# Optimization experiments

Measured on AMD Instinct MI355X. Metric: run time of the kernel, lower is better.

Reference implementation:

```python
import jax, jax.numpy as jnp
import numpy as np

NC = 6          # num_classes
KP = 8          # num_prototype_per_class
NPROTO = NC * KP
PH, PW = 4, 4   # patch grid (num_h, num_w)
MOM = 0.999
EPS = 1e-6


def _layernorm(x, g, b):
    mu = jnp.mean(x, axis=-1, keepdims=True)
    var = jnp.var(x, axis=-1, keepdims=True)
    return (x - mu) / jnp.sqrt(var + EPS) * g + b


def _patch_split(x, nh, nw):
    # (B,C,H,W) -> (B*nh*nw, C, H//nh, W//nw)
    B, C, H, W = x.shape
    ph, pw = H // nh, W // nw
    x = x.reshape(B, C, nh, ph, nw, pw).transpose(0, 2, 4, 1, 3, 5)
    return x.reshape(B * nh * nw, C, ph, pw)


def setup_inputs() -> dict:
    key = jax.random.key(0)
    k1, k2, k3 = jax.random.split(key, 3)
    B, C, Hh, Wh = 8, 128, 128, 128
    Horg, Worg = 512, 512
    return {
        "feats": jax.random.normal(k1, (B, C, Hh, Wh), dtype=jnp.float32),
        "gt": jax.random.randint(k2, (B, Horg, Worg), 0, 7, dtype=jnp.int64),
        "prototype": jax.random.normal(k3, (NPROTO, C), dtype=jnp.float32),
        "ln1_gamma": jnp.ones((C,), jnp.float32),
        "ln1_beta": jnp.zeros((C,), jnp.float32),
        "ln2_gamma": jnp.ones((NPROTO,), jnp.float32),
        "ln2_beta": jnp.zeros((NPROTO,), jnp.float32),
    }


def reference(feats, gt, prototype, ln1_gamma, ln1_beta, ln2_gamma, ln2_beta):
    B, C, Hh, Wh = feats.shape
    Horg, Worg = gt.shape[1], gt.shape[2]

    # --- nearest-neighbor downsample of gt to head resolution (torch 'nearest')
    ih = (jnp.arange(Hh) * Horg) // Hh
    iw = (jnp.arange(Wh) * Worg) // Wh
    label = gt[:, ih[:, None], iw[None, :]]                      # (B,Hh,Wh)
    mask = (label.astype(jnp.int32) != NC).astype(label.dtype)
    one_hot = jax.nn.one_hot(label * mask, NC, dtype=jnp.float32)  # (B,Hh,Wh,NC)
    # torch code does a raw .view(B,-1,Hh,Wh) on the contiguous one-hot; replicate
    pred0 = one_hot.reshape(B, NC, Hh, Wh)

    # --- patch split + spatial gather (softmax-weighted class centers per patch)
    pf = _patch_split(feats, PH, PW)                             # (B*16, C, ph, pw)
    pp = _patch_split(pred0, PH, PW)                             # (B*16, NC, ph, pw)
    bp = pf.shape[0]
    probs = jax.nn.softmax(pp.reshape(bp, NC, -1), axis=2)       # (B*16, NC, HWp)
    fflat = pf.reshape(bp, C, -1)                                # (B*16, C, HWp)
    ctx = jnp.einsum('bkn,bcn->bkc', probs, fflat)               # (B*16, NC, C)

    centers = ctx.reshape(B, PH * PW, NC, C)
    centers = jax.nn.gelu(_layernorm(centers, ln1_gamma, ln1_beta), approximate=False)
    centers = centers.reshape(B, PH * PW * NC, C)                # (B, 96, C)

    # --- nearest prototype assignment (cdist + argmin)
    c2 = jnp.sum(centers * centers, axis=-1)                     # (B,96)
    p2 = jnp.sum(prototype * prototype, axis=-1)                 # (48,)
    d2 = c2[:, :, None] + p2[None, None, :] - 2.0 * jnp.einsum('bmc,kc->bmk', centers, prototype)
    nearest = jnp.argmin(jnp.sqrt(jnp.maximum(d2, 0.0)), axis=-1)  # (B,96)

    # --- sequential, order-dependent momentum EMA scatter update (training path)
    sg = jax.lax.stop_gradient
    idx_flat = nearest.reshape(-1)
    ctr_flat = sg(centers.reshape(-1, C))

    def step(proto, xs):
        i, v = xs
        nv = MOM * proto[i] + (1.0 - MOM) * v
        return proto.at[i].set(nv), None

    proto_val, _ = jax.lax.scan(step, sg(prototype), (idx_flat, ctr_flat))
    # in torch the update writes .data (no grad); downstream grad w.r.t. prototype is identity
    proto_new = prototype + sg(proto_val - prototype)

    # --- prototype-to-pixel cdist similarity map
    nf = feats.reshape(B, C, -1).transpose(0, 2, 1)              # (B,HW,C)
    f2 = jnp.sum(nf * nf, axis=-1)                               # (B,HW)
    pn2 = jnp.sum(proto_new * proto_new, axis=-1)                # (48,)
    d2b = pn2[None, :, None] + f2[:, None, :] - 2.0 * jnp.einsum('kc,bnc->bkn', proto_new, nf)
    distance_l2 = jnp.sqrt(jnp.maximum(d2b, 0.0))                # (B,48,HW)

    p2c = (1.0 / (1.0 + 2.0 * distance_l2)).reshape(B, NPROTO, Hh, Wh)
    p2c = p2c.transpose(0, 2, 3, 1)
    p2c = jax.nn.gelu(_layernorm(p2c, ln2_gamma, ln2_beta), approximate=False)
    p2c_sim_map = p2c.transpose(0, 3, 1, 2)                      # (B,48,Hh,Wh)

    pred = p2c_sim_map.reshape(B, KP, NC, Hh, Wh).max(axis=1)    # (B,NC,Hh,Wh)
    pred = jax.image.resize(pred, (B, NC, Horg, Worg), method='bilinear')

    prototype_expand = jnp.broadcast_to(proto_new, (B, NPROTO, C))
    return pred, prototype_expand, p2c_sim_map, distance_l2, proto_new
```

## Files before the change

kernel.cpp:

```cpp
#include <hip/hip_runtime.h>
#include <hip/hip_bf16.h>
#include <math.h>


#define E_M1 1.71828182845904523536f
#define INV_SQRT2 0.70710678118654752440f

typedef float v2f __attribute__((ext_vector_type(2)));

__device__ __forceinline__ float gelu_exact(float x) {
    return 0.5f * x * (1.f + erff(x * INV_SQRT2));
}
__device__ __forceinline__ v2f splat2(float x) { v2f r; r.x = x; r.y = x; return r; }

__global__ __launch_bounds__(256) void kern0b(const int* __restrict__ gt,
                                              unsigned char* __restrict__ maskb) {
    int idx = blockIdx.x * 256 + threadIdx.x;
    int b = idx >> 14, P = idx & 16383;
    const int* gb = gt + b * 262144;
    unsigned int m = 0;
    #pragma unroll
    for (int c = 0; c < 6; ++c) {
        int pos = c * 16384 + P;
        int hp = pos / 768;
        int rem = pos - hp * 768;
        int wp = rem / 6;
        int kp = rem - wp * 6;
        int g = gb[(4 * hp) * 512 + 4 * wp];
        int lab = (g == 6) ? 0 : g;
        if (lab == kp) m |= (1u << c);
    }
    maskb[idx] = (unsigned char)m;
}

__global__ __launch_bounds__(256) void kernA1(
    const float* __restrict__ feats, const unsigned char* __restrict__ maskb,
    float* __restrict__ part)
{
    __shared__ float accs[7][128];
    const int pidx = blockIdx.x;
    const int patch = pidx >> 2, q = pidx & 3;
    const int b = patch >> 4, pp = patch & 15, ihh = pp >> 2, iww = pp & 3;
    const int c = threadIdx.x & 127, sub = threadIdx.x >> 7;

    const int row0 = ihh * 32 + q * 8 + sub * 4;
    const float* fb = feats + (((long long)(b * 128 + c)) * 128 + row0) * 128 + iww * 32;
    const unsigned char* mb = maskb + b * 16384 + row0 * 128 + iww * 32;

    float s0 = 0.f, s1 = 0.f, s2 = 0.f, s3 = 0.f, s4 = 0.f, s5 = 0.f, sall = 0.f;
    for (int r = 0; r < 4; ++r) {
        const float4* row = (const float4*)(fb + r * 128);
        const unsigned int* mr = (const unsigned int*)(mb + r * 128);
        #pragma unroll
        for (int j = 0; j < 8; ++j) {
            float4 v = row[j];
            unsigned int u = mr[j];
            unsigned int b0 = u, b1 = u >> 8, b2 = u >> 16, b3 = u >> 24;
            s0 += ((b0 >> 0) & 1) ? v.x : 0.f;  s1 += ((b0 >> 1) & 1) ? v.x : 0.f;
            s2 += ((b0 >> 2) & 1) ? v.x : 0.f;  s3 += ((b0 >> 3) & 1) ? v.x : 0.f;
            s4 += ((b0 >> 4) & 1) ? v.x : 0.f;  s5 += ((b0 >> 5) & 1) ? v.x : 0.f;
            s0 += ((b1 >> 0) & 1) ? v.y : 0.f;  s1 += ((b1 >> 1) & 1) ? v.y : 0.f;
            s2 += ((b1 >> 2) & 1) ? v.y : 0.f;  s3 += ((b1 >> 3) & 1) ? v.y : 0.f;
            s4 += ((b1 >> 4) & 1) ? v.y : 0.f;  s5 += ((b1 >> 5) & 1) ? v.y : 0.f;
            s0 += ((b2 >> 0) & 1) ? v.z : 0.f;  s1 += ((b2 >> 1) & 1) ? v.z : 0.f;
            s2 += ((b2 >> 2) & 1) ? v.z : 0.f;  s3 += ((b2 >> 3) & 1) ? v.z : 0.f;
            s4 += ((b2 >> 4) & 1) ? v.z : 0.f;  s5 += ((b2 >> 5) & 1) ? v.z : 0.f;
            s0 += ((b3 >> 0) & 1) ? v.w : 0.f;  s1 += ((b3 >> 1) & 1) ? v.w : 0.f;
            s2 += ((b3 >> 2) & 1) ? v.w : 0.f;  s3 += ((b3 >> 3) & 1) ? v.w : 0.f;
            s4 += ((b3 >> 4) & 1) ? v.w : 0.f;  s5 += ((b3 >> 5) & 1) ? v.w : 0.f;
            sall += v.x + v.y + v.z + v.w;
        }
    }
    if (sub == 1) {
        accs[0][c] = s0; accs[1][c] = s1; accs[2][c] = s2; accs[3][c] = s3;
        accs[4][c] = s4; accs[5][c] = s5; accs[6][c] = sall;
    }
    __syncthreads();
    if (sub == 0) {
        float* po = part + pidx * 896;
        po[0 * 128 + c] = s0 + accs[0][c];
        po[1 * 128 + c] = s1 + accs[1][c];
        po[2 * 128 + c] = s2 + accs[2][c];
        po[3 * 128 + c] = s3 + accs[3][c];
        po[4 * 128 + c] = s4 + accs[4][c];
        po[5 * 128 + c] = s5 + accs[5][c];
        po[6 * 128 + c] = sall + accs[6][c];
    }
}

__global__ __launch_bounds__(512) void kernA2(
    const float* __restrict__ part, const unsigned char* __restrict__ maskb,
    const float* __restrict__ proto,
    const float* __restrict__ g1, const float* __restrict__ b1,
    float* __restrict__ centersT, int* __restrict__ nearest)
{
    __shared__ float ct[6][128];
    __shared__ int cnt[6];
    __shared__ float pl[48 * 129];

    const int tid = threadIdx.x;
    const int p = blockIdx.x;
    const int b = p >> 4, pp = p & 15, ihh = pp >> 2, iww = pp & 3;

    if (tid < 6) cnt[tid] = 0;
    for (int i = tid; i < 6144; i += 512)
        pl[(i >> 7) * 129 + (i & 127)] = proto[i];
    __syncthreads();

    if (tid < 256) {
        const unsigned char* mb = maskb + b * 16384 + ihh * 32 * 128 + iww * 32;
        int r = tid >> 3, jw = tid & 7;
        unsigned int u = *(const unsigned int*)(mb + r * 128 + jw * 4);
        #pragma unroll
        for (int k = 0; k < 6; ++k) {
            int cc = ((u >> k) & 1) + ((u >> (8 + k)) & 1) +
                     ((u >> (16 + k)) & 1) + ((u >> (24 + k)) & 1);
            #pragma unroll
            for (int m = 1; m < 64; m <<= 1) cc += __shfl_xor(cc, m, 64);
            if ((tid & 63) == 0 && cc) atomicAdd(&cnt[k], cc);
        }
    }
    __syncthreads();

    const float* pb = part + (p * 4) * 896;
    for (int i = tid; i < 768; i += 512) {
        const int c = i & 127, k = i >> 7;
        float Sall = pb[6 * 128 + c] + pb[896 + 6 * 128 + c] +
                     pb[2 * 896 + 6 * 128 + c] + pb[3 * 896 + 6 * 128 + c];
        float Sk = pb[k * 128 + c] + pb[896 + k * 128 + c] +
                   pb[2 * 896 + k * 128 + c] + pb[3 * 896 + k * 128 + c];
        float Z = fmaf((float)cnt[k], E_M1, 1024.f);
        ct[k][c] = (Sall + E_M1 * Sk) / Z;
    }
    __syncthreads();

    const int wv = tid >> 6, lane = tid & 63;
    if (wv < 6) {
        float x0 = ct[wv][lane], x1 = ct[wv][lane + 64];
        float s = x0 + x1;
        #pragma unroll
        for (int m = 1; m < 64; m <<= 1) s += __shfl_xor(s, m, 64);
        float mu = s * (1.f / 128.f);
        float d0 = x0 - mu, d1 = x1 - mu;
        float ss = d0 * d0 + d1 * d1;
        #pragma unroll
        for (int m = 1; m < 64; m <<= 1) ss += __shfl_xor(ss, m, 64);
        float inv = 1.f / sqrtf(ss * (1.f / 128.f) + 1e-6f);
        float y0 = d0 * inv * g1[lane] + b1[lane];
        float y1 = d1 * inv * g1[lane + 64] + b1[lane + 64];
        float z0 = gelu_exact(y0);
        float z1 = gelu_exact(y1);
        const int row = (b * 16 + pp) * 6 + wv;
        centersT[lane * 768 + row] = z0;
        centersT[(lane + 64) * 768 + row] = z1;

        float best = INFINITY; int bi = 0;
        for (int k = 0; k < 48; ++k) {
            float t0 = z0 - pl[k * 129 + lane];
            float t1 = z1 - pl[k * 129 + 64 + lane];
            float sd = fmaf(t0, t0, t1 * t1);
            #pragma unroll
            for (int m = 1; m < 64; m <<= 1) sd += __shfl_xor(sd, m, 64);
            if (sd < best) { best = sd; bi = k; }
        }
        if (lane == 0) nearest[row] = bi;
    }
}

__global__ __launch_bounds__(128) void kernD(
    const float* __restrict__ proto0, const int* __restrict__ nearest,
    const float* __restrict__ centersT,
    float* __restrict__ proto_new, float* __restrict__ pn2,
    float* __restrict__ out_expand, float* __restrict__ out_proto)
{
    __shared__ int nl[768];
    __shared__ float wred[2];
    const int k = blockIdx.x, c = threadIdx.x;
    for (int i = c; i < 768; i += 128) nl[i] = nearest[i];
    __syncthreads();
    float p = proto0[k * 128 + c];
    const float OM = (float)(1.0 - 0.999);
    const float* col = centersT + c * 768;
    #pragma unroll 4
    for (int i = 0; i < 768; i += 4) {
        float4 v = *(const float4*)(col + i);
        if (nl[i + 0] == k) p = 0.999f * p + OM * v.x;
        if (nl[i + 1] == k) p = 0.999f * p + OM * v.y;
        if (nl[i + 2] == k) p = 0.999f * p + OM * v.z;
        if (nl[i + 3] == k) p = 0.999f * p + OM * v.w;
    }
    proto_new[k * 128 + c] = p;
    out_proto[k * 128 + c] = p;
    #pragma unroll
    for (int b = 0; b < 8; ++b) out_expand[(b * 48 + k) * 128 + c] = p;
    float sq = p * p;
    #pragma unroll
    for (int m = 1; m < 64; m <<= 1) sq += __shfl_xor(sq, m, 64);
    if ((c & 63) == 0) wred[c >> 6] = sq;
    __syncthreads();
    if (c == 0) pn2[k] = wred[0] + wred[1];
}

__global__ __launch_bounds__(512, 4) void kernE(
    const float* __restrict__ feats, const float* __restrict__ proto_new,
    const float* __restrict__ pn2g,
    const float* __restrict__ g2, const float* __restrict__ b2,
    float* __restrict__ out_sim, float* __restrict__ out_dist,
    float* __restrict__ pred_small)
{
    __shared__ float smem[16264];
    float* prot = smem;
    float* red  = smem;
    float* dst  = smem + 12936;
    float* F2   = smem + 16072;
    float* muv  = smem + 16136;
    float* invv = smem + 16200;
    float* lnA  = smem;
    float* lnB  = smem + 256;

    const int t = threadIdx.x;
    const int b = blockIdx.y;
    const int nbase = blockIdx.x * 64;

    for (int i4 = t; i4 < 1536; i4 += 512) {
        float4 v = ((const float4*)proto_new)[i4];
        *(float4*)&prot[(i4 >> 5) * 132 + (i4 & 31) * 4] = v;
    }
    __syncthreads();

    const int w = t >> 6, l = t & 63;
    const int cw = w & 3, nh = w >> 2;
    const int n0 = nh * 32 + (l & 7) * 4;
    const int k0 = (l >> 3) * 6;
    const int cbase = cw * 32;

    const float* fb = feats + (((long long)b) << 21) + (cbase << 14) + nbase + n0;

    v2f acc[6][2];
    #pragma unroll
    for (int j = 0; j < 6; ++j) { acc[j][0] = splat2(0.f); acc[j][1] = splat2(0.f); }
    v2f aF0 = splat2(0.f), aF1 = splat2(0.f);

    #pragma unroll
    for (int cq = 0; cq < 8; ++cq) {
        const int cb = cbase + cq * 4;
        v2f f[4][2];
        #pragma unroll
        for (int ch = 0; ch < 4; ++ch) {
            float4 a = *(const float4*)(fb + ((cq * 4 + ch) << 14));
            f[ch][0] = *(v2f*)&a.x; f[ch][1] = *(v2f*)&a.z;
        }
        #pragma unroll
        for (int j = 0; j < 6; ++j) {
            float4 pv = *(const float4*)&prot[(k0 + j) * 132 + cb];
            v2f px = splat2(pv.x), py = splat2(pv.y), pz = splat2(pv.z), pw = splat2(pv.w);
            #pragma unroll
            for (int h = 0; h < 2; ++h) {
                acc[j][h] = __builtin_elementwise_fma(f[0][h], px,
                            __builtin_elementwise_fma(f[1][h], py,
                            __builtin_elementwise_fma(f[2][h], pz,
                            __builtin_elementwise_fma(f[3][h], pw, acc[j][h]))));
            }
        }
        aF0 = __builtin_elementwise_fma(f[0][0], f[0][0],
              __builtin_elementwise_fma(f[1][0], f[1][0],
              __builtin_elementwise_fma(f[2][0], f[2][0],
              __builtin_elementwise_fma(f[3][0], f[3][0], aF0))));
        aF1 = __builtin_elementwise_fma(f[0][1], f[0][1],
              __builtin_elementwise_fma(f[1][1], f[1][1],
              __builtin_elementwise_fma(f[2][1], f[2][1],
              __builtin_elementwise_fma(f[3][1], f[3][1], aF1))));
    }
    __syncthreads();

    #pragma unroll
    for (int j = 0; j < 6; ++j) {
        *(v2f*)&red[cw * 3234 + (k0 + j) * 66 + n0]     = acc[j][0];
        *(v2f*)&red[cw * 3234 + (k0 + j) * 66 + n0 + 2] = acc[j][1];
    }
    if (l < 8) {
        *(v2f*)&red[cw * 3234 + 3168 + n0]     = aF0;
        *(v2f*)&red[cw * 3234 + 3168 + n0 + 2] = aF1;
    }
    __syncthreads();

    if (t < 64)
        F2[t] = ((red[3168 + t] + red[3234 + 3168 + t]) +
                 red[2 * 3234 + 3168 + t]) + red[3 * 3234 + 3168 + t];
    __syncthreads();

    for (int cell = t; cell < 768; cell += 512) {
        const int k = cell >> 4, n4 = (cell & 15) * 4;
        v2f lo = splat2(0.f), hi = splat2(0.f);
        #pragma unroll
        for (int ww = 0; ww < 4; ++ww) {
            lo += *(const v2f*)&red[ww * 3234 + k * 66 + n4];
            hi += *(const v2f*)&red[ww * 3234 + k * 66 + n4 + 2];
        }
        float pk = pn2g[k];
        float d0 = sqrtf(fmaxf(F2[n4 + 0] + pk - 2.f * lo.x, 0.f));
        float d1 = sqrtf(fmaxf(F2[n4 + 1] + pk - 2.f * lo.y, 0.f));
        float d2 = sqrtf(fmaxf(F2[n4 + 2] + pk - 2.f * hi.x, 0.f));
        float d3 = sqrtf(fmaxf(F2[n4 + 3] + pk - 2.f * hi.y, 0.f));
        float4 dv; dv.x = d0; dv.y = d1; dv.z = d2; dv.w = d3;
        *(float4*)(out_dist + (((long long)(b * 48 + k)) << 14) + nbase + n4) = dv;
        dst[(n4 + 0) * 49 + k] = 1.f / (1.f + 2.f * d0);
        dst[(n4 + 1) * 49 + k] = 1.f / (1.f + 2.f * d1);
        dst[(n4 + 2) * 49 + k] = 1.f / (1.f + 2.f * d2);
        dst[(n4 + 3) * 49 + k] = 1.f / (1.f + 2.f * d3);
    }
    __syncthreads();

    if (t < 256) {
        const int n = t & 63, q = t >> 6;
        float s1 = 0.f, s2 = 0.f;
        for (int k = q * 12; k < q * 12 + 12; ++k) {
            float x = dst[n * 49 + k];
            s1 += x; s2 = fmaf(x, x, s2);
        }
        lnA[q * 64 + n] = s1;
        lnB[q * 64 + n] = s2;
    }
    __syncthreads();
    if (t < 64) {
        float s1 = ((lnA[t] + lnA[64 + t]) + lnA[128 + t]) + lnA[192 + t];
        float s2 = ((lnB[t] + lnB[64 + t]) + lnB[128 + t]) + lnB[192 + t];
        float mu = s1 * (1.f / 48.f);
        float var = fmaxf(s2 * (1.f / 48.f) - mu * mu, 0.f);
        muv[t] = mu;
        invv[t] = 1.f / sqrtf(var + 1e-6f);
    }
    __syncthreads();

    if (t < 384) {
        const int c6 = t >> 6, n = t & 63, ng = nbase + n;
        float mu = muv[n], inv = invv[n];
        float pm = 0.f;
        #pragma unroll
        for (int kp = 0; kp < 8; ++kp) {
            int k = kp * 6 + c6;
            float y = (dst[n * 49 + k] - mu) * inv * g2[k] + b2[k];
            float z = gelu_exact(y);
            out_sim[(((long long)(b * 48 + k)) << 14) + ng] = z;
            pm = (kp == 0) ? z : fmaxf(pm, z);
        }
        pred_small[((b * 6 + c6) << 14) + ng] = pm;
    }
}

__global__ __launch_bounds__(256) void kernF(
    const float* __restrict__ ps, float* __restrict__ pred)
{
    int idx = blockIdx.x * 256 + threadIdx.x;
    int xq = idx & 127;
    int oy = (idx >> 7) & 511;
    int bc = idx >> 16;
    int qy = oy >> 2, ry = oy & 3;
    int y0 = qy + ((ry < 2) ? -1 : 0);
    float fy = (ry == 0) ? 0.625f : (ry == 1) ? 0.875f : (ry == 2) ? 0.125f : 0.375f;
    int y0c = max(y0, 0), y1c = min(y0 + 1, 127);
    const float* base = ps + bc * 16384;
    const float* rA = base + y0c * 128;
    const float* rB = base + y1c * 128;
    int xm = max(xq - 1, 0), xp = min(xq + 1, 127);
    float a0 = rA[xm], a1 = rA[xq], a2 = rA[xp];
    float c0 = rB[xm], c1 = rB[xq], c2 = rB[xp];
    float w0 = 1.f - fy;
    float gm = w0 * a0 + fy * c0;
    float gc = w0 * a1 + fy * c1;
    float gp = w0 * a2 + fy * c2;
    float4 o;
    o.x = 0.375f * gm + 0.625f * gc;
    o.y = 0.125f * gm + 0.875f * gc;
    o.z = 0.875f * gc + 0.125f * gp;
    o.w = 0.625f * gc + 0.375f * gp;
    *(float4*)(pred + ((long long)idx << 2)) = o;
}

extern "C" void kernel_launch(void* const* d_in, const int* in_sizes, int n_in,
                              void* d_out, int out_size, void* d_ws, size_t ws_size,
                              hipStream_t stream)
{
    const float* feats = (const float*)d_in[0];
    const int* gt = (const int*)d_in[1];
    const float* proto = (const float*)d_in[2];
    const float* g1 = (const float*)d_in[3];
    const float* b1 = (const float*)d_in[4];
    const float* g2 = (const float*)d_in[5];
    const float* b2 = (const float*)d_in[6];

    float* out = (float*)d_out;
    float* pred       = out;
    float* out_expand = out + 12582912;
    float* out_sim    = out + 12632064;
    float* out_dist   = out + 18923520;
    float* out_proto  = out + 25214976;

    float* ws = (float*)d_ws;
    float* centersT   = ws + 98304;
    float* proto_new  = ws + 196608;
    float* pn2        = ws + 202752;
    int*   nearest    = (int*)(ws + 202816);
    float* part       = ws + 203584;
    float* pred_small = ws + 203584;
    unsigned char* maskb = (unsigned char*)(ws + 990016);

    kern0b<<<512, 256, 0, stream>>>(gt, maskb);
    kernA1<<<512, 256, 0, stream>>>(feats, maskb, part);
    kernA2<<<128, 512, 0, stream>>>(part, maskb, proto, g1, b1, centersT, nearest);
    kernD <<<48, 128, 0, stream>>>(proto, nearest, centersT, proto_new, pn2,
                                   out_expand, out_proto);
    kernE <<<dim3(256, 8), 512, 0, stream>>>(feats, proto_new, pn2, g2, b2,
                                             out_sim, out_dist, pred_small);
    kernF <<<12288, 256, 0, stream>>>(pred_small, pred);
}
```

Measured before the change: 294.0 us.

## Stage feature tiles in LDS via async global_load_lds and widen kernA1 blocks

In the distance kernel, the block's 128x64 feature tile is now copied straight into shared memory with global_load_lds before the FMA loop. Threads then read their operands from LDS instead of issuing strided per-channel global loads. kernA1 is widened to 512 threads, with each thread covering 2 rows instead of 4, and three shared partial sets are summed at the end. The kernE occupancy hint is dropped. The changes trade shared-memory pressure and register or occupancy changes for better load coalescing and more parallelism in the reduction.

```diff
diff --git a/kernel.cpp b/kernel.cpp
--- a/kernel.cpp
+++ b/kernel.cpp
@@ -12,6 +12,12 @@
     return 0.5f * x * (1.f + erff(x * INV_SQRT2));
 }
 __device__ __forceinline__ v2f splat2(float x) { v2f r; r.x = x; r.y = x; return r; }
+
+__device__ __forceinline__ void gload16(const float* g, float* l) {
+    __builtin_amdgcn_global_load_lds(
+        (const __attribute__((address_space(1))) void*)g,
+        (__attribute__((address_space(3))) void*)l, 16, 0, 0);
+}
 
 __global__ __launch_bounds__(256) void kern0b(const int* __restrict__ gt,
                                               unsigned char* __restrict__ maskb) {
@@ -33,22 +39,22 @@
     maskb[idx] = (unsigned char)m;
 }
 
-__global__ __launch_bounds__(256) void kernA1(
+__global__ __launch_bounds__(512) void kernA1(
     const float* __restrict__ feats, const unsigned char* __restrict__ maskb,
     float* __restrict__ part)
 {
-    __shared__ float accs[7][128];
+    __shared__ float accs[3][7][128];
     const int pidx = blockIdx.x;
     const int patch = pidx >> 2, q = pidx & 3;
     const int b = patch >> 4, pp = patch & 15, ihh = pp >> 2, iww = pp & 3;
     const int c = threadIdx.x & 127, sub = threadIdx.x >> 7;
 
-    const int row0 = ihh * 32 + q * 8 + sub * 4;
+    const int row0 = ihh * 32 + q * 8 + sub * 2;
     const float* fb = feats + (((long long)(b * 128 + c)) * 128 + row0) * 128 + iww * 32;
     const unsigned char* mb = maskb + b * 16384 + row0 * 128 + iww * 32;
 
     float s0 = 0.f, s1 = 0.f, s2 = 0.f, s3 = 0.f, s4 = 0.f, s5 = 0.f, sall = 0.f;
-    for (int r = 0; r < 4; ++r) {
+    for (int r = 0; r < 2; ++r) {
         const float4* row = (const float4*)(fb + r * 128);
         const unsigned int* mr = (const unsigned int*)(mb + r * 128);
         #pragma unroll
@@ -71,20 +77,22 @@
             sall += v.x + v.y + v.z + v.w;
         }
     }
-    if (sub == 1) {
-        accs[0][c] = s0; accs[1][c] = s1; accs[2][c] = s2; accs[3][c] = s3;
-        accs[4][c] = s4; accs[5][c] = s5; accs[6][c] = sall;
+    if (sub > 0) {
+        float* a = &accs[sub - 1][0][0];
+        a[0 * 128 + c] = s0; a[1 * 128 + c] = s1; a[2 * 128 + c] = s2;
+        a[3 * 128 + c] = s3; a[4 * 128 + c] = s4; a[5 * 128 + c] = s5;
+        a[6 * 128 + c] = sall;
     }
     __syncthreads();
     if (sub == 0) {
         float* po = part + pidx * 896;
-        po[0 * 128 + c] = s0 + accs[0][c];
-        po[1 * 128 + c] = s1 + accs[1][c];
-        po[2 * 128 + c] = s2 + accs[2][c];
-        po[3 * 128 + c] = s3 + accs[3][c];
-        po[4 * 128 + c] = s4 + accs[4][c];
-        po[5 * 128 + c] = s5 + accs[5][c];
-        po[6 * 128 + c] = sall + accs[6][c];
+        po[0 * 128 + c] = s0 + accs[0][0][c] + accs[1][0][c] + accs[2][0][c];
+        po[1 * 128 + c] = s1 + accs[0][1][c] + accs[1][1][c] + accs[2][1][c];
+        po[2 * 128 + c] = s2 + accs[0][2][c] + accs[1][2][c] + accs[2][2][c];
+        po[3 * 128 + c] = s3 + accs[0][3][c] + accs[1][3][c] + accs[2][3][c];
+        po[4 * 128 + c] = s4 + accs[0][4][c] + accs[1][4][c] + accs[2][4][c];
+        po[5 * 128 + c] = s5 + accs[0][5][c] + accs[1][5][c] + accs[2][5][c];
+        po[6 * 128 + c] = sall + accs[0][6][c] + accs[1][6][c] + accs[2][6][c];
     }
 }
 
@@ -201,7 +209,7 @@
     if (c == 0) pn2[k] = wred[0] + wred[1];
 }
 
-__global__ __launch_bounds__(512, 4) void kernE(
+__global__ __launch_bounds__(512) void kernE(
     const float* __restrict__ feats, const float* __restrict__ proto_new,
     const float* __restrict__ pn2g,
     const float* __restrict__ g2, const float* __restrict__ b2,
@@ -209,7 +217,8 @@
     float* __restrict__ pred_small)
 {
     __shared__ float smem[16264];
-    float* prot = smem;
+    float* fT   = smem;
+    float* prot = smem + 8192;
     float* red  = smem;
     float* dst  = smem + 12936;
     float* F2   = smem + 16072;
@@ -222,6 +231,13 @@
     const int b = blockIdx.y;
     const int nbase = blockIdx.x * 64;
 
+    #pragma unroll
+    for (int it = 0; it < 4; ++it) {
+        int idx = it * 512 + t;
+        int c = idx >> 4, qd = idx & 15;
+        gload16(feats + (((long long)(b * 128 + c)) << 14) + nbase + qd * 4,
+                &fT[idx * 4]);
+    }
     for (int i4 = t; i4 < 1536; i4 += 512) {
         float4 v = ((const float4*)proto_new)[i4];
         *(float4*)&prot[(i4 >> 5) * 132 + (i4 & 31) * 4] = v;
@@ -234,8 +250,6 @@
     const int k0 = (l >> 3) * 6;
     const int cbase = cw * 32;
 
-    const float* fb = feats + (((long long)b) << 21) + (cbase << 14) + nbase + n0;
-
     v2f acc[6][2];
     #pragma unroll
     for (int j = 0; j < 6; ++j) { acc[j][0] = splat2(0.f); acc[j][1] = splat2(0.f); }
@@ -247,8 +261,8 @@
         v2f f[4][2];
         #pragma unroll
         for (int ch = 0; ch < 4; ++ch) {
-            float4 a = *(const float4*)(fb + ((cq * 4 + ch) << 14));
-            f[ch][0] = *(v2f*)&a.x; f[ch][1] = *(v2f*)&a.z;
+            float4 a0 = *(const float4*)&fT[(cb + ch) * 64 + n0];
+            f[ch][0] = *(v2f*)&a0.x; f[ch][1] = *(v2f*)&a0.z;
         }
         #pragma unroll
         for (int j = 0; j < 6; ++j) {
@@ -406,11 +420,11 @@
     unsigned char* maskb = (unsigned char*)(ws + 990016);
 
     kern0b<<<512, 256, 0, stream>>>(gt, maskb);
-    kernA1<<<512, 256, 0, stream>>>(feats, maskb, part);
+    kernA1<<<512, 512, 0, stream>>>(feats, maskb, part);
     kernA2<<<128, 512, 0, stream>>>(part, maskb, proto, g1, b1, centersT, nearest);
     kernD <<<48, 128, 0, stream>>>(proto, nearest, centersT, proto_new, pn2,
                                    out_expand, out_proto);
     kernE <<<dim3(256, 8), 512, 0, stream>>>(feats, proto_new, pn2, g2, b2,
                                              out_sim, out_dist, pred_small);
-    kernF <<<12288, 256, 0, stream>>>(pred_small, pred);
-}
+    kernF<<<12288, 256, 0, stream>>>(pred_small, pred);
+}
```

Result: faster. 280.5 us (-4.6%).
